# Kernel tuning notes

Measured on AMD Instinct MI355X. Metric: run time of the kernel, lower is better.

Reference implementation:

```python
import jax, jax.numpy as jnp
import numpy as np


def _gru_cell(x, h, Wih, Whh):
    # PyTorch GRU (bias=False): gates ordered [r, z, n] along rows of W.
    gi = x @ Wih.T              # [B, 3H]
    gh = h @ Whh.T              # [B, 3H]
    ir, iz, inn = jnp.split(gi, 3, axis=-1)
    hr, hz, hn = jnp.split(gh, 3, axis=-1)
    r = jax.nn.sigmoid(ir + hr)
    z = jax.nn.sigmoid(iz + hz)
    n = jnp.tanh(inn + r * hn)
    return (1.0 - z) * n + z * h


def setup_inputs() -> dict:
    key = jax.random.key(0)
    ks = jax.random.split(key, 16)
    B, T = 256, 1024
    U, Z, Y, H = 16, 16, 16, 128
    W = 0.1  # weight scale for stable recurrence
    inp = {
        "u": jax.random.normal(ks[0], (B, U, T), jnp.float32),
        "y": jax.random.normal(ks[1], (B, Y, T), jnp.float32),
        "h0": jax.random.uniform(ks[2], (2, B, H), jnp.float32),
        "Wih0": W * jax.random.normal(ks[3], (3 * H, U + Z), jnp.float32),
        "Whh0": W * jax.random.normal(ks[4], (3 * H, H), jnp.float32),
        "Wih1": W * jax.random.normal(ks[5], (3 * H, H), jnp.float32),
        "Whh1": W * jax.random.normal(ks[6], (3 * H, H), jnp.float32),
        "dW1": W * jax.random.normal(ks[7], (H, U + H), jnp.float32),
        "db1": jnp.zeros((H,), jnp.float32),
        "dW2": W * jax.random.normal(ks[8], (Z, H), jnp.float32),
        "db2": jnp.zeros((Z,), jnp.float32),
        "mW1": W * jax.random.normal(ks[9], (H, Z + H), jnp.float32),
        "mb1": jnp.zeros((H,), jnp.float32),
        "mW2": W * jax.random.normal(ks[10], (H, H), jnp.float32),
        "mb2": jnp.zeros((H,), jnp.float32),
        "mW3": W * jax.random.normal(ks[11], (Y, H), jnp.float32),
        "mb3": jnp.zeros((Y,), jnp.float32),
    }
    return inp


def reference(u, y, h0, Wih0, Whh0, Wih1, Whh1,
              dW1, db1, dW2, db2, mW1, mb1, mW2, mb2, mW3, mb3):
    B, Z = u.shape[0], dW2.shape[0]
    u_t = jnp.transpose(u, (2, 0, 1))  # [T, B, U]
    y_t = jnp.transpose(y, (2, 0, 1))  # [T, B, Y]

    def step(carry, xs):
        h, x_prev, loss = carry  # h: [2, B, H]
        ut, yt = xs
        inp = jnp.concatenate([ut, x_prev], axis=1)       # [B, U+Z]
        h0n = _gru_cell(inp, h[0], Wih0, Whh0)
        h1n = _gru_cell(h0n, h[1], Wih1, Whh1)
        h_new = jnp.stack([h0n, h1n], axis=0)
        # dynn: two Linears, no activation; input cat(u_t, h[-1])
        d_in = jnp.concatenate([ut, h1n], axis=1)         # [B, U+H]
        x_t = (d_in @ dW1.T + db1) @ dW2.T + db2          # [B, Z]
        # menn: Linear -> ReLU -> Linear -> Linear; input cat(x_t, h[0])
        m_in = jnp.concatenate([x_t, h0n], axis=1)        # [B, Z+H]
        m = jax.nn.relu(m_in @ mW1.T + mb1)
        m = m @ mW2.T + mb2
        y_hat = m @ mW3.T + mb3                           # [B, Y]
        loss = loss + jnp.sum((y_hat - yt) ** 2)
        return (h_new, x_t, loss), None

    x0 = jnp.zeros((B, Z), jnp.float32)  # x_tm1 at t=0 is zeros
    (_, _, loss), _ = jax.lax.scan(step, (h0, x0, jnp.float32(0.0)), (u_t, y_t))
    return loss
```

## Files before the change

### kernel.cpp

```cpp
#include <hip/hip_runtime.h>

typedef __bf16 bf16x8 __attribute__((ext_vector_type(8)));
typedef float f32x4 __attribute__((ext_vector_type(4)));
typedef unsigned int uint32;
typedef unsigned short u16;

#define T_STEPS 1024
#define CH_STR 784

#define H0_OFF   0
#define H1_OFF   8704
#define M1_OFF   17408
#define UCH_OFF  21760
#define YCH_OFF  46848
#define WL_OFF   71936
#define LDS_BYTES 146688

#define TG0 0
#define TG1 24
#define TG2 120
#define TG3 216
#define TG4 312
#define TG5 317
#define TG6 357
#define NT_TOT 361
#define SC_DC  369664
#define SC_ME  378880
#define SC_DBC 387072
#define SC_MBE 387136

static __device__ __forceinline__ u16 f2bf(float f) {
    uint32 u = __builtin_bit_cast(uint32, f);
    return (u16)((u + 0x7FFFu + ((u >> 16) & 1u)) >> 16);
}
static __device__ __forceinline__ float bf2f(u16 h) {
    uint32 u = ((uint32)h) << 16;
    return __builtin_bit_cast(float, u);
}
static __device__ __forceinline__ uint32 cvtpk(float a, float b) {
    uint32 r;
    asm("v_cvt_pk_bf16_f32 %0, %1, %2" : "=v"(r) : "v"(a), "v"(b));
    return r;
}
static __device__ __forceinline__ float sigm(float x) {
    return __builtin_amdgcn_rcpf(1.f + __builtin_amdgcn_exp2f(x * -1.4426950408889634f));
}
static __device__ __forceinline__ float tanh_fast(float x) {
    float xm = fmaxf(x, -30.f);
    float e = __builtin_amdgcn_exp2f(xm * -2.8853900817779268f);
    return fmaf(2.f, __builtin_amdgcn_rcpf(e + 1.f), -1.f);
}
static __device__ __forceinline__ f32x4 mfma16(bf16x8 a, bf16x8 b, f32x4 c) {
    return __builtin_amdgcn_mfma_f32_16x16x32_bf16(a, b, c, 0, 0, 0);
}
static __device__ __forceinline__ bf16x8 ldsAF(const char* p) {
    return __builtin_bit_cast(bf16x8, *(const uint4*)p);
}

__global__ void prep1(const float* __restrict__ dW1, const float* __restrict__ db1,
                      const float* __restrict__ dW2, const float* __restrict__ db2,
                      const float* __restrict__ mW2, const float* __restrict__ mb2,
                      const float* __restrict__ mW3, const float* __restrict__ mb3,
                      char* __restrict__ ws, float* __restrict__ out) {
    int id = blockIdx.x * 256 + threadIdx.x;
    if (id == 0) *out = 0.f;
    if (id < 2304) {
        int n = id / 144, k = id % 144;
        float s = 0.f;
        for (int h = 0; h < 128; ++h) s += dW2[n * 128 + h] * dW1[h * 144 + k];
        ((float*)(ws + SC_DC))[id] = s;
    } else if (id < 4352) {
        int e = id - 2304, n = e / 128, k = e % 128;
        float s = 0.f;
        for (int h = 0; h < 128; ++h) s += mW3[n * 128 + h] * mW2[h * 128 + k];
        ((float*)(ws + SC_ME))[e] = s;
    } else if (id < 4368) {
        int n = id - 4352;
        float s = db2[n];
        for (int h = 0; h < 128; ++h) s += dW2[n * 128 + h] * db1[h];
        ((float*)(ws + SC_DBC))[n] = s;
    } else if (id < 4384) {
        int n = id - 4368;
        float s = mb3[n];
        for (int h = 0; h < 128; ++h) s += mW3[n * 128 + h] * mb2[h];
        ((float*)(ws + SC_MBE))[n] = s;
    }
}

__global__ void prep2(const float* __restrict__ W0, const float* __restrict__ W1,
                      const float* __restrict__ W2, const float* __restrict__ W3,
                      const float* __restrict__ W5, char* __restrict__ ws) {
    const int tt = blockIdx.x;
    const int lane = threadIdx.x;
    const int cum[8] = {TG0, TG1, TG2, TG3, TG4, TG5, TG6, NT_TOT};
    const int Kreal[7] = {32, 128, 128, 128, 144, 144, 128};
    const int KT[7] = {1, 4, 4, 4, 5, 5, 4};
    const float* Ws[7] = {W0, W1, W2, W3, (const float*)(ws + SC_DC), W5, (const float*)(ws + SC_ME)};
    int g = 0;
    while (tt >= cum[g + 1]) ++g;
    const int tl = tt - cum[g];
    const int kt = tl % KT[g];
    const int n = (tl / KT[g]) * 16 + (lane & 15);
    const float* W = Ws[g];
    u16* o = (u16*)ws + tt * 512 + lane * 8;
#pragma unroll
    for (int j = 0; j < 8; ++j) {
        int k = kt * 32 + (lane >> 4) * 8 + j;
        o[j] = (k < Kreal[g]) ? f2bf(W[n * Kreal[g] + k]) : (u16)0;
    }
}

__global__ __launch_bounds__(512, 2) void rnn_main(
    const float* __restrict__ u, const float* __restrict__ yg, const float* __restrict__ h0g,
    const char* __restrict__ ws, const float* __restrict__ mb1g,
    const float* __restrict__ dbCg, const float* __restrict__ mbEg,
    float* __restrict__ out) {
    __shared__ __align__(16) char smem[LDS_BYTES];
    const int tid = threadIdx.x;
    const int lane = tid & 63;
    const int w = tid >> 6;
    const int lr = lane & 15;
    const int lg = lane >> 4;
    const int r0 = blockIdx.x * 16;
    const uint4* F4 = (const uint4*)ws;
    const f32x4 zero = {0.f, 0.f, 0.f, 0.f};

    for (int i = tid; i < 1024; i += 512) {
        int lay = i >> 9, rem = i & 511, rr = rem >> 5, k4 = rem & 31;
        float4 v = *(const float4*)(h0g + (lay * 256 + r0 + rr) * 128 + k4 * 4);
        uint2 pk;
        pk.x = (uint32)f2bf(v.x) | ((uint32)f2bf(v.y) << 16);
        pk.y = (uint32)f2bf(v.z) | ((uint32)f2bf(v.w) << 16);
        *(uint2*)(smem + H0_OFF + lay * 8704 + rr * 272 + k4 * 8) = pk;
    }
    for (int i = tid; i < 73 * 64; i += 512) {
        int li = i >> 6, ln2 = i & 63;
        int gt2 = (li < 24) ? li : (li < 29) ? TG4 + (li - 24) : (li < 69) ? TG5 + (li - 29) : TG6 + (li - 69);
        *((uint4*)(smem + WL_OFF) + i) = F4[gt2 * 64 + ln2];
    }
    __syncthreads();

    bf16x8 wW[3][3][4];
    for (int p = 0; p < 6; ++p) {
        for (int i = tid; i < 3072; i += 512)
            *((uint4*)(smem + UCH_OFF) + i) = F4[(TG1 + p * 48) * 64 + i];
        __syncthreads();
#pragma unroll
        for (int mat = 0; mat < 3; ++mat)
#pragma unroll
            for (int gg = 0; gg < 3; ++gg) {
                int rel0 = mat * 96 + gg * 32 + w * 4;
                if (rel0 >= p * 48 && rel0 < p * 48 + 48) {
#pragma unroll
                    for (int kt = 0; kt < 4; ++kt)
                        wW[mat][gg][kt] = ldsAF(smem + UCH_OFF + (rel0 - p * 48 + kt) * 1024 + lane * 16);
                }
            }
        __syncthreads();
    }

    const float mb1_c = mb1g[w * 16 + lr];
    const float mbE_l = mbEg[lr];
    float dbc4[4];
#pragma unroll
    for (int i = 0; i < 4; ++i) dbc4[i] = dbCg[lg * 4 + i];
    float hp0[4], hp1[4];
#pragma unroll
    for (int i = 0; i < 4; ++i) {
        hp0[i] = h0g[(r0 + lg * 4 + i) * 128 + w * 16 + lr];
        hp1[i] = h0g[(256 + r0 + lg * 4 + i) * 128 + w * 16 + lr];
    }
    float loss = 0.f;
    const int c2 = (w * 16 + lr) * 2;
    const int bp0 = (lr + (lg & 1) * 32) * 4;

    for (int t = 0; t < T_STEPS; ++t) {
        const char* h0c = smem + H0_OFF + (t & 1) * 4352;
        char* h0n = smem + H0_OFF + ((t & 1) ^ 1) * 4352;
        const char* h1c = smem + H1_OFF + (t & 1) * 4352;
        char* h1n = smem + H1_OFF + ((t & 1) ^ 1) * 4352;
        const int s = t & 31, sp = (t - 1) & 31;
        const char* h1r = h1c + lr * 272;

        bf16x8 ad0 = ldsAF((lg < 2) ? (smem + UCH_OFF + sp * CH_STR + lr * 48 + lg * 16)
                                    : (h1r + (lg - 2) * 16));
        bf16x8 ad1 = ldsAF(h1r + 32 + lg * 16);
        bf16x8 ad2 = ldsAF(h1r + 96 + lg * 16);
        bf16x8 ad3 = ldsAF(h1r + 160 + lg * 16);
        bf16x8 ad4 = ldsAF(h1r + 224 + (lg & 1) * 16);
        f32x4 xa = mfma16(ldsAF(smem + WL_OFF + 24 * 1024 + lane * 16), ad0, zero);
        xa = mfma16(ldsAF(smem + WL_OFF + 25 * 1024 + lane * 16), ad1, xa);
        xa = mfma16(ldsAF(smem + WL_OFF + 26 * 1024 + lane * 16), ad2, xa);
        f32x4 xb = mfma16(ldsAF(smem + WL_OFF + 27 * 1024 + lane * 16), ad3, zero);
        xb = mfma16(ldsAF(smem + WL_OFF + 28 * 1024 + lane * 16), ad4, xb);
        uint32 pk0 = cvtpk(xa[0] + xb[0] + dbc4[0], xa[1] + xb[1] + dbc4[1]);
        uint32 pk1 = cvtpk(xa[2] + xb[2] + dbc4[2], xa[3] + xb[3] + dbc4[3]);
        if (t == 0) { pk0 = 0u; pk1 = 0u; }
        uint32 d0 = (uint32)__builtin_amdgcn_ds_bpermute(bp0, (int)pk0);
        uint32 d1 = (uint32)__builtin_amdgcn_ds_bpermute(bp0, (int)pk1);
        uint32 d2 = (uint32)__builtin_amdgcn_ds_bpermute(bp0 + 64, (int)pk0);
        uint32 d3 = (uint32)__builtin_amdgcn_ds_bpermute(bp0 + 64, (int)pk1);
        bf16x8 xfrag = __builtin_bit_cast(bf16x8, (uint4){d0, d1, d2, d3});

        if ((t & 31) == 0) {
            __syncthreads();
#pragma unroll
            for (int it = 0; it < 8; ++it) {
                int g = it * 16 + (tid >> 5);
                int rr2 = g >> 3, chp = g & 7, ss = lane & 31;
                const float* up = u + (r0 + rr2) * 16384 + (2 * chp) * 1024 + t + ss;
                *(uint32*)(smem + UCH_OFF + ss * CH_STR + rr2 * 48 + chp * 4) =
                    cvtpk(up[0], up[1024]);
                int gt = t - 1 + ss;
                const float* yp = yg + (r0 + rr2) * 16384 + (2 * chp) * 1024 + gt;
                uint32 py = (gt >= 0) ? cvtpk(yp[0], yp[1024]) : 0u;
                *(uint32*)(smem + YCH_OFF + ss * CH_STR + rr2 * 48 + chp * 4) = py;
            }
            __syncthreads();
        }

        bf16x8 ufrag = ldsAF(smem + UCH_OFF + s * CH_STR + lr * 48 + (lg & 1) * 16);
        bf16x8 a_inp = (lg < 2) ? ufrag : xfrag;
        const char* h0r = h0c + lr * 272;
        bf16x8 ah0 = ldsAF(h0r + lg * 16);
        bf16x8 ah1 = ldsAF(h0r + 64 + lg * 16);
        bf16x8 ah2 = ldsAF(h0r + 128 + lg * 16);
        bf16x8 ah3 = ldsAF(h0r + 192 + lg * 16);
        bf16x8 b0r = ldsAF(smem + WL_OFF + (0 * 8 + w) * 1024 + lane * 16);
        bf16x8 b0z = ldsAF(smem + WL_OFF + (1 * 8 + w) * 1024 + lane * 16);
        bf16x8 b0n = ldsAF(smem + WL_OFF + (2 * 8 + w) * 1024 + lane * 16);
        f32x4 rA = mfma16(ah0, wW[0][0][0], zero);
        rA = mfma16(ah1, wW[0][0][1], rA);
        rA = mfma16(a_inp, b0r, rA);
        f32x4 rB = mfma16(ah2, wW[0][0][2], zero);
        rB = mfma16(ah3, wW[0][0][3], rB);
        f32x4 zA = mfma16(ah0, wW[0][1][0], zero);
        zA = mfma16(ah1, wW[0][1][1], zA);
        zA = mfma16(a_inp, b0z, zA);
        f32x4 zB = mfma16(ah2, wW[0][1][2], zero);
        zB = mfma16(ah3, wW[0][1][3], zB);
        f32x4 nI = mfma16(a_inp, b0n, zero);
        f32x4 nA = mfma16(ah0, wW[0][2][0], zero);
        nA = mfma16(ah1, wW[0][2][1], nA);
        f32x4 nB = mfma16(ah2, wW[0][2][2], zero);
        nB = mfma16(ah3, wW[0][2][3], nB);
        bf16x8 am0 = (lg < 2) ? xfrag : ldsAF(h0r + (lg - 2) * 16);
        bf16x8 am1 = ldsAF(h0r + 32 + lg * 16);
        bf16x8 am2 = ldsAF(h0r + 96 + lg * 16);
        bf16x8 am3 = ldsAF(h0r + 160 + lg * 16);
        bf16x8 am4 = ldsAF(h0r + 224 + (lg & 1) * 16);
        const int mb = 29 + w * 5;
        f32x4 mA = mfma16(am1, ldsAF(smem + WL_OFF + (mb + 1) * 1024 + lane * 16), zero);
        mA = mfma16(am2, ldsAF(smem + WL_OFF + (mb + 2) * 1024 + lane * 16), mA);
        mA = mfma16(am0, ldsAF(smem + WL_OFF + (mb + 0) * 1024 + lane * 16), mA);
        f32x4 mB = mfma16(am3, ldsAF(smem + WL_OFF + (mb + 3) * 1024 + lane * 16), zero);
        mB = mfma16(am4, ldsAF(smem + WL_OFF + (mb + 4) * 1024 + lane * 16), mB);
#pragma unroll
        for (int i = 0; i < 4; ++i) {
            float rr = sigm(rA[i] + rB[i]);
            float zz = sigm(zA[i] + zB[i]);
            float nn = tanh_fast(fmaf(rr, nA[i] + nB[i], nI[i]));
            float hnew = fmaf(zz, hp0[i] - nn, nn);
            hp0[i] = hnew;
            *(u16*)(h0n + (lg * 4 + i) * 272 + c2) = (u16)cvtpk(hnew, hnew);
            float mv = fmaxf(mA[i] + mB[i] + mb1_c, 0.f);
            *(u16*)(smem + M1_OFF + (lg * 4 + i) * 272 + c2) = (u16)cvtpk(mv, mv);
        }
        __syncthreads();

        const char* h0nr = h0n + lr * 272;
        bf16x8 ag0 = ldsAF(h0nr + lg * 16);
        bf16x8 ag1 = ldsAF(h0nr + 64 + lg * 16);
        bf16x8 ag2 = ldsAF(h0nr + 128 + lg * 16);
        bf16x8 ag3 = ldsAF(h0nr + 192 + lg * 16);
        bf16x8 av0 = ldsAF(h1r + lg * 16);
        bf16x8 av1 = ldsAF(h1r + 64 + lg * 16);
        bf16x8 av2 = ldsAF(h1r + 128 + lg * 16);
        bf16x8 av3 = ldsAF(h1r + 192 + lg * 16);
        bf16x8 q0, q1, q2, q3, we0, we1, we2, we3;
        if (w == 7) {
            const char* m1r = smem + M1_OFF + lr * 272;
            q0 = ldsAF(m1r + lg * 16);
            q1 = ldsAF(m1r + 64 + lg * 16);
            q2 = ldsAF(m1r + 128 + lg * 16);
            q3 = ldsAF(m1r + 192 + lg * 16);
            we0 = ldsAF(smem + WL_OFF + 69 * 1024 + lane * 16);
            we1 = ldsAF(smem + WL_OFF + 70 * 1024 + lane * 16);
            we2 = ldsAF(smem + WL_OFF + 71 * 1024 + lane * 16);
            we3 = ldsAF(smem + WL_OFF + 72 * 1024 + lane * 16);
        }
        f32x4 bRi = mfma16(ag0, wW[1][0][0], zero);
        bRi = mfma16(ag1, wW[1][0][1], bRi);
        bRi = mfma16(ag2, wW[1][0][2], bRi);
        bRi = mfma16(ag3, wW[1][0][3], bRi);
        f32x4 bRh = mfma16(av0, wW[2][0][0], zero);
        bRh = mfma16(av1, wW[2][0][1], bRh);
        bRh = mfma16(av2, wW[2][0][2], bRh);
        bRh = mfma16(av3, wW[2][0][3], bRh);
        f32x4 bZi = mfma16(ag0, wW[1][1][0], zero);
        bZi = mfma16(ag1, wW[1][1][1], bZi);
        bZi = mfma16(ag2, wW[1][1][2], bZi);
        bZi = mfma16(ag3, wW[1][1][3], bZi);
        f32x4 bZh = mfma16(av0, wW[2][1][0], zero);
        bZh = mfma16(av1, wW[2][1][1], bZh);
        bZh = mfma16(av2, wW[2][1][2], bZh);
        bZh = mfma16(av3, wW[2][1][3], bZh);
        f32x4 bNi = mfma16(ag0, wW[1][2][0], zero);
        bNi = mfma16(ag1, wW[1][2][1], bNi);
        bNi = mfma16(ag2, wW[1][2][2], bNi);
        bNi = mfma16(ag3, wW[1][2][3], bNi);
        f32x4 bNh = mfma16(av0, wW[2][2][0], zero);
        bNh = mfma16(av1, wW[2][2][1], bNh);
        bNh = mfma16(av2, wW[2][2][2], bNh);
        bNh = mfma16(av3, wW[2][2][3], bNh);
        if (w == 7) {
            f32x4 lA = mfma16(q0, we0, zero);
            lA = mfma16(q1, we1, lA);
            f32x4 lB = mfma16(q2, we2, zero);
            lB = mfma16(q3, we3, lB);
            const float gd = (t > 0) ? 1.f : 0.f;
#pragma unroll
            for (int i = 0; i < 4; ++i) {
                float yh = lA[i] + lB[i] + mbE_l;
                float yv = bf2f(*(const u16*)(smem + YCH_OFF + s * CH_STR + (lg * 4 + i) * 48 + lr * 2));
                float d = yh - yv;
                loss = fmaf(gd * d, d, loss);
            }
        }
#pragma unroll
        for (int i = 0; i < 4; ++i) {
            float rr = sigm(bRi[i] + bRh[i]);
            float zz = sigm(bZi[i] + bZh[i]);
            float nn = tanh_fast(fmaf(rr, bNh[i], bNi[i]));
            float hnew = fmaf(zz, hp1[i] - nn, nn);
            hp1[i] = hnew;
            *(u16*)(h1n + (lg * 4 + i) * 272 + c2) = (u16)cvtpk(hnew, hnew);
        }
        __syncthreads();
    }

    {
        const char* h0c = smem + H0_OFF;
        const char* h1c = smem + H1_OFF;
        const char* h1r = h1c + lr * 272;
        const char* h0r = h0c + lr * 272;
        bf16x8 ad0 = ldsAF((lg < 2) ? (smem + UCH_OFF + 31 * CH_STR + lr * 48 + lg * 16)
                                    : (h1r + (lg - 2) * 16));
        bf16x8 ad1 = ldsAF(h1r + 32 + lg * 16);
        bf16x8 ad2 = ldsAF(h1r + 96 + lg * 16);
        bf16x8 ad3 = ldsAF(h1r + 160 + lg * 16);
        bf16x8 ad4 = ldsAF(h1r + 224 + (lg & 1) * 16);
        f32x4 xa = mfma16(ldsAF(smem + WL_OFF + 24 * 1024 + lane * 16), ad0, zero);
        xa = mfma16(ldsAF(smem + WL_OFF + 25 * 1024 + lane * 16), ad1, xa);
        xa = mfma16(ldsAF(smem + WL_OFF + 26 * 1024 + lane * 16), ad2, xa);
        f32x4 xb = mfma16(ldsAF(smem + WL_OFF + 27 * 1024 + lane * 16), ad3, zero);
        xb = mfma16(ldsAF(smem + WL_OFF + 28 * 1024 + lane * 16), ad4, xb);
        uint32 pk0 = cvtpk(xa[0] + xb[0] + dbc4[0], xa[1] + xb[1] + dbc4[1]);
        uint32 pk1 = cvtpk(xa[2] + xb[2] + dbc4[2], xa[3] + xb[3] + dbc4[3]);
        uint32 d0 = (uint32)__builtin_amdgcn_ds_bpermute(bp0, (int)pk0);
        uint32 d1 = (uint32)__builtin_amdgcn_ds_bpermute(bp0, (int)pk1);
        uint32 d2 = (uint32)__builtin_amdgcn_ds_bpermute(bp0 + 64, (int)pk0);
        uint32 d3 = (uint32)__builtin_amdgcn_ds_bpermute(bp0 + 64, (int)pk1);
        bf16x8 xfrag = __builtin_bit_cast(bf16x8, (uint4){d0, d1, d2, d3});
        bf16x8 am0 = (lg < 2) ? xfrag : ldsAF(h0r + (lg - 2) * 16);
        bf16x8 am1 = ldsAF(h0r + 32 + lg * 16);
        bf16x8 am2 = ldsAF(h0r + 96 + lg * 16);
        bf16x8 am3 = ldsAF(h0r + 160 + lg * 16);
        bf16x8 am4 = ldsAF(h0r + 224 + (lg & 1) * 16);
        const int mb = 29 + w * 5;
        f32x4 m = mfma16(am0, ldsAF(smem + WL_OFF + (mb + 0) * 1024 + lane * 16), zero);
        m = mfma16(am1, ldsAF(smem + WL_OFF + (mb + 1) * 1024 + lane * 16), m);
        m = mfma16(am2, ldsAF(smem + WL_OFF + (mb + 2) * 1024 + lane * 16), m);
        m = mfma16(am3, ldsAF(smem + WL_OFF + (mb + 3) * 1024 + lane * 16), m);
        m = mfma16(am4, ldsAF(smem + WL_OFF + (mb + 4) * 1024 + lane * 16), m);
#pragma unroll
        for (int i = 0; i < 4; ++i) {
            float mv = fmaxf(m[i] + mb1_c, 0.f);
            *(u16*)(smem + M1_OFF + (lg * 4 + i) * 272 + c2) = (u16)cvtpk(mv, mv);
        }
        __syncthreads();
        if (w == 7) {
            const char* m1r = smem + M1_OFF + lr * 272;
            bf16x8 q0 = ldsAF(m1r + lg * 16);
            bf16x8 q1 = ldsAF(m1r + 64 + lg * 16);
            bf16x8 q2 = ldsAF(m1r + 128 + lg * 16);
            bf16x8 q3 = ldsAF(m1r + 192 + lg * 16);
            f32x4 lA = mfma16(q0, ldsAF(smem + WL_OFF + 69 * 1024 + lane * 16), zero);
            lA = mfma16(q1, ldsAF(smem + WL_OFF + 70 * 1024 + lane * 16), lA);
            f32x4 lB = mfma16(q2, ldsAF(smem + WL_OFF + 71 * 1024 + lane * 16), zero);
            lB = mfma16(q3, ldsAF(smem + WL_OFF + 72 * 1024 + lane * 16), lB);
#pragma unroll
            for (int i = 0; i < 4; ++i) {
                float yh = lA[i] + lB[i] + mbE_l;
                float yv = yg[(r0 + lg * 4 + i) * 16384 + lr * 1024 + 1023];
                float d = yh - yv;
                loss = fmaf(d, d, loss);
            }
        }
    }

    if (w == 7) {
#pragma unroll
        for (int off = 32; off > 0; off >>= 1) loss += __shfl_down(loss, off, 64);
        if (lane == 0) atomicAdd(out, loss);
    }
}

extern "C" void kernel_launch(void* const* d_in, const int* in_sizes, int n_in,
                              void* d_out, int out_size, void* d_ws, size_t ws_size,
                              hipStream_t stream) {
    const float* u    = (const float*)d_in[0];
    const float* y    = (const float*)d_in[1];
    const float* h0   = (const float*)d_in[2];
    const float* Wih0 = (const float*)d_in[3];
    const float* Whh0 = (const float*)d_in[4];
    const float* Wih1 = (const float*)d_in[5];
    const float* Whh1 = (const float*)d_in[6];
    const float* dW1  = (const float*)d_in[7];
    const float* db1  = (const float*)d_in[8];
    const float* dW2  = (const float*)d_in[9];
    const float* db2  = (const float*)d_in[10];
    const float* mW1  = (const float*)d_in[11];
    const float* mb1  = (const float*)d_in[12];
    const float* mW2  = (const float*)d_in[13];
    const float* mb2  = (const float*)d_in[14];
    const float* mW3  = (const float*)d_in[15];
    const float* mb3  = (const float*)d_in[16];
    float* out = (float*)d_out;
    char* ws = (char*)d_ws;

    prep1<<<dim3(18), dim3(256), 0, stream>>>(dW1, db1, dW2, db2, mW2, mb2, mW3, mb3, ws, out);
    prep2<<<dim3(NT_TOT), dim3(64), 0, stream>>>(Wih0, Whh0, Wih1, Whh1, mW1, ws);
    rnn_main<<<dim3(16), dim3(512), 0, stream>>>(u, y, h0, ws, mb1,
                                                 (const float*)(ws + SC_DBC),
                                                 (const float*)(ws + SC_MBE), out);
}
```

Baseline: 3.053 ms.

## Swap MFMA operand order to produce transposed outputs and vectorize LDS stores

Swaps the A/B operands of every MFMA so each lane's four accumulator values fall along the hidden dimension for one batch row instead of along the batch dimension. This lets the new h0, h1 and menn hidden values be packed into a single 8-byte LDS store per lane rather than four scalar 2-byte stores. Biases and the initial hidden state are loaded as float4 to match the new mapping, and the y chunk loss read becomes one vector load. The u/y chunk staging loop is rewritten to store one bf16 per element with a tighter stride of 768, which adds more global loads and narrower stores in the refill every 32 steps.

Result: slower. 4.439 ms (+45.4%).

```diff
diff --git a/kernel.cpp b/kernel.cpp
--- a/kernel.cpp
+++ b/kernel.cpp
@@ -6,15 +6,15 @@
 typedef unsigned short u16;
 
 #define T_STEPS 1024
-#define CH_STR 784
+#define CH_STR 768
 
 #define H0_OFF   0
 #define H1_OFF   8704
 #define M1_OFF   17408
 #define UCH_OFF  21760
-#define YCH_OFF  46848
-#define WL_OFF   71936
-#define LDS_BYTES 146688
+#define YCH_OFF  46336
+#define WL_OFF   70912
+#define LDS_BYTES 145664
 
 #define TG0 0
 #define TG1 24
@@ -159,20 +159,31 @@
         __syncthreads();
     }
 
-    const float mb1_c = mb1g[w * 16 + lr];
-    const float mbE_l = mbEg[lr];
-    float dbc4[4];
-#pragma unroll
-    for (int i = 0; i < 4; ++i) dbc4[i] = dbCg[lg * 4 + i];
+    float mb1_4[4], dbc4[4], mbe4[4];
+    {
+        float4 t1 = *(const float4*)(mb1g + w * 16 + lg * 4);
+        float4 t2 = *(const float4*)(dbCg + lg * 4);
+        float4 t3 = *(const float4*)(mbEg + lg * 4);
+#pragma unroll
+        for (int i = 0; i < 4; ++i) {
+            mb1_4[i] = ((const float*)&t1)[i];
+            dbc4[i] = ((const float*)&t2)[i];
+            mbe4[i] = ((const float*)&t3)[i];
+        }
+    }
     float hp0[4], hp1[4];
-#pragma unroll
-    for (int i = 0; i < 4; ++i) {
-        hp0[i] = h0g[(r0 + lg * 4 + i) * 128 + w * 16 + lr];
-        hp1[i] = h0g[(256 + r0 + lg * 4 + i) * 128 + w * 16 + lr];
+    {
+        float4 t1 = *(const float4*)(h0g + (r0 + lr) * 128 + w * 16 + lg * 4);
+        float4 t2 = *(const float4*)(h0g + (256 + r0 + lr) * 128 + w * 16 + lg * 4);
+#pragma unroll
+        for (int i = 0; i < 4; ++i) {
+            hp0[i] = ((const float*)&t1)[i];
+            hp1[i] = ((const float*)&t2)[i];
+        }
     }
     float loss = 0.f;
-    const int c2 = (w * 16 + lr) * 2;
-    const int bp0 = (lr + (lg & 1) * 32) * 4;
+    const int cb = w * 32 + lg * 8;
+    const int bp0 = ((lg & 1) * 32 + lr) * 4;
 
     for (int t = 0; t < T_STEPS; ++t) {
         const char* h0c = smem + H0_OFF + (t & 1) * 4352;
@@ -204,17 +215,16 @@
 
         if ((t & 31) == 0) {
             __syncthreads();
-#pragma unroll
-            for (int it = 0; it < 8; ++it) {
-                int g = it * 16 + (tid >> 5);
-                int rr2 = g >> 3, chp = g & 7, ss = lane & 31;
-                const float* up = u + (r0 + rr2) * 16384 + (2 * chp) * 1024 + t + ss;
-                *(uint32*)(smem + UCH_OFF + ss * CH_STR + rr2 * 48 + chp * 4) =
-                    cvtpk(up[0], up[1024]);
+            for (int q = 0; q < 16; ++q) {
+                int pair = w * 32 + q * 2 + (lane >> 5);
+                int rr2 = pair >> 4, ch = pair & 15, ss = lane & 31;
+                float v = u[(r0 + rr2) * 16384 + ch * 1024 + t + ss];
+                *(u16*)(smem + UCH_OFF + ss * CH_STR + rr2 * 48 + ch * 2) = f2bf(v);
                 int gt = t - 1 + ss;
-                const float* yp = yg + (r0 + rr2) * 16384 + (2 * chp) * 1024 + gt;
-                uint32 py = (gt >= 0) ? cvtpk(yp[0], yp[1024]) : 0u;
-                *(uint32*)(smem + YCH_OFF + ss * CH_STR + rr2 * 48 + chp * 4) = py;
+                if (gt >= 0) {
+                    float vy = yg[(r0 + rr2) * 16384 + ch * 1024 + gt];
+                    *(u16*)(smem + YCH_OFF + ss * CH_STR + rr2 * 48 + ch * 2) = f2bf(vy);
+                }
             }
             __syncthreads();
         }
@@ -229,42 +239,50 @@
         bf16x8 b0r = ldsAF(smem + WL_OFF + (0 * 8 + w) * 1024 + lane * 16);
         bf16x8 b0z = ldsAF(smem + WL_OFF + (1 * 8 + w) * 1024 + lane * 16);
         bf16x8 b0n = ldsAF(smem + WL_OFF + (2 * 8 + w) * 1024 + lane * 16);
-        f32x4 rA = mfma16(ah0, wW[0][0][0], zero);
-        rA = mfma16(ah1, wW[0][0][1], rA);
-        rA = mfma16(a_inp, b0r, rA);
-        f32x4 rB = mfma16(ah2, wW[0][0][2], zero);
-        rB = mfma16(ah3, wW[0][0][3], rB);
-        f32x4 zA = mfma16(ah0, wW[0][1][0], zero);
-        zA = mfma16(ah1, wW[0][1][1], zA);
-        zA = mfma16(a_inp, b0z, zA);
-        f32x4 zB = mfma16(ah2, wW[0][1][2], zero);
-        zB = mfma16(ah3, wW[0][1][3], zB);
-        f32x4 nI = mfma16(a_inp, b0n, zero);
-        f32x4 nA = mfma16(ah0, wW[0][2][0], zero);
-        nA = mfma16(ah1, wW[0][2][1], nA);
-        f32x4 nB = mfma16(ah2, wW[0][2][2], zero);
-        nB = mfma16(ah3, wW[0][2][3], nB);
+        f32x4 rA = mfma16(wW[0][0][0], ah0, zero);
+        rA = mfma16(wW[0][0][1], ah1, rA);
+        rA = mfma16(b0r, a_inp, rA);
+        f32x4 rB = mfma16(wW[0][0][2], ah2, zero);
+        rB = mfma16(wW[0][0][3], ah3, rB);
+        f32x4 zA = mfma16(wW[0][1][0], ah0, zero);
+        zA = mfma16(wW[0][1][1], ah1, zA);
+        zA = mfma16(b0z, a_inp, zA);
+        f32x4 zB = mfma16(wW[0][1][2], ah2, zero);
+        zB = mfma16(wW[0][1][3], ah3, zB);
+        f32x4 nI = mfma16(b0n, a_inp, zero);
+        f32x4 nA = mfma16(wW[0][2][0], ah0, zero);
+        nA = mfma16(wW[0][2][1], ah1, nA);
+        f32x4 nB = mfma16(wW[0][2][2], ah2, zero);
+        nB = mfma16(wW[0][2][3], ah3, nB);
         bf16x8 am0 = (lg < 2) ? xfrag : ldsAF(h0r + (lg - 2) * 16);
         bf16x8 am1 = ldsAF(h0r + 32 + lg * 16);
         bf16x8 am2 = ldsAF(h0r + 96 + lg * 16);
         bf16x8 am3 = ldsAF(h0r + 160 + lg * 16);
         bf16x8 am4 = ldsAF(h0r + 224 + (lg & 1) * 16);
         const int mb = 29 + w * 5;
-        f32x4 mA = mfma16(am1, ldsAF(smem + WL_OFF + (mb + 1) * 1024 + lane * 16), zero);
-        mA = mfma16(am2, ldsAF(smem + WL_OFF + (mb + 2) * 1024 + lane * 16), mA);
-        mA = mfma16(am0, ldsAF(smem + WL_OFF + (mb + 0) * 1024 + lane * 16), mA);
-        f32x4 mB = mfma16(am3, ldsAF(smem + WL_OFF + (mb + 3) * 1024 + lane * 16), zero);
-        mB = mfma16(am4, ldsAF(smem + WL_OFF + (mb + 4) * 1024 + lane * 16), mB);
+        f32x4 mA = mfma16(ldsAF(smem + WL_OFF + (mb + 1) * 1024 + lane * 16), am1, zero);
+        mA = mfma16(ldsAF(smem + WL_OFF + (mb + 2) * 1024 + lane * 16), am2, mA);
+        mA = mfma16(ldsAF(smem + WL_OFF + (mb + 0) * 1024 + lane * 16), am0, mA);
+        f32x4 mB = mfma16(ldsAF(smem + WL_OFF + (mb + 3) * 1024 + lane * 16), am3, zero);
+        mB = mfma16(ldsAF(smem + WL_OFF + (mb + 4) * 1024 + lane * 16), am4, mB);
+        float hn0[4];
 #pragma unroll
         for (int i = 0; i < 4; ++i) {
             float rr = sigm(rA[i] + rB[i]);
             float zz = sigm(zA[i] + zB[i]);
             float nn = tanh_fast(fmaf(rr, nA[i] + nB[i], nI[i]));
-            float hnew = fmaf(zz, hp0[i] - nn, nn);
-            hp0[i] = hnew;
-            *(u16*)(h0n + (lg * 4 + i) * 272 + c2) = (u16)cvtpk(hnew, hnew);
-            float mv = fmaxf(mA[i] + mB[i] + mb1_c, 0.f);
-            *(u16*)(smem + M1_OFF + (lg * 4 + i) * 272 + c2) = (u16)cvtpk(mv, mv);
+            hn0[i] = fmaf(zz, hp0[i] - nn, nn);
+            hp0[i] = hn0[i];
+        }
+        {
+            uint2 hv = {cvtpk(hn0[0], hn0[1]), cvtpk(hn0[2], hn0[3])};
+            *(uint2*)(h0n + lr * 272 + cb) = hv;
+            float m0 = fmaxf(mA[0] + mB[0] + mb1_4[0], 0.f);
+            float m1v = fmaxf(mA[1] + mB[1] + mb1_4[1], 0.f);
+            float m2v = fmaxf(mA[2] + mB[2] + mb1_4[2], 0.f);
+            float m3v = fmaxf(mA[3] + mB[3] + mb1_4[3], 0.f);
+            uint2 mv = {cvtpk(m0, m1v), cvtpk(m2v, m3v)};
+            *(uint2*)(smem + M1_OFF + lr * 272 + cb) = mv;
         }
         __syncthreads();
 
@@ -289,52 +307,57 @@
             we2 = ldsAF(smem + WL_OFF + 71 * 1024 + lane * 16);
             we3 = ldsAF(smem + WL_OFF + 72 * 1024 + lane * 16);
         }
-        f32x4 bRi = mfma16(ag0, wW[1][0][0], zero);
-        bRi = mfma16(ag1, wW[1][0][1], bRi);
-        bRi = mfma16(ag2, wW[1][0][2], bRi);
-        bRi = mfma16(ag3, wW[1][0][3], bRi);
-        f32x4 bRh = mfma16(av0, wW[2][0][0], zero);
-        bRh = mfma16(av1, wW[2][0][1], bRh);
-        bRh = mfma16(av2, wW[2][0][2], bRh);
-        bRh = mfma16(av3, wW[2][0][3], bRh);
-        f32x4 bZi = mfma16(ag0, wW[1][1][0], zero);
-        bZi = mfma16(ag1, wW[1][1][1], bZi);
-        bZi = mfma16(ag2, wW[1][1][2], bZi);
-        bZi = mfma16(ag3, wW[1][1][3], bZi);
-        f32x4 bZh = mfma16(av0, wW[2][1][0], zero);
-        bZh = mfma16(av1, wW[2][1][1], bZh);
-        bZh = mfma16(av2, wW[2][1][2], bZh);
-        bZh = mfma16(av3, wW[2][1][3], bZh);
-        f32x4 bNi = mfma16(ag0, wW[1][2][0], zero);
-        bNi = mfma16(ag1, wW[1][2][1], bNi);
-        bNi = mfma16(ag2, wW[1][2][2], bNi);
-        bNi = mfma16(ag3, wW[1][2][3], bNi);
-        f32x4 bNh = mfma16(av0, wW[2][2][0], zero);
-        bNh = mfma16(av1, wW[2][2][1], bNh);
-        bNh = mfma16(av2, wW[2][2][2], bNh);
-        bNh = mfma16(av3, wW[2][2][3], bNh);
+        f32x4 bRi = mfma16(wW[1][0][0], ag0, zero);
+        bRi = mfma16(wW[1][0][1], ag1, bRi);
+        bRi = mfma16(wW[1][0][2], ag2, bRi);
+        bRi = mfma16(wW[1][0][3], ag3, bRi);
+        f32x4 bRh = mfma16(wW[2][0][0], av0, zero);
+        bRh = mfma16(wW[2][0][1], av1, bRh);
+        bRh = mfma16(wW[2][0][2], av2, bRh);
+        bRh = mfma16(wW[2][0][3], av3, bRh);
+        f32x4 bZi = mfma16(wW[1][1][0], ag0, zero);
+        bZi = mfma16(wW[1][1][1], ag1, bZi);
+        bZi = mfma16(wW[1][1][2], ag2, bZi);
+        bZi = mfma16(wW[1][1][3], ag3, bZi);
+        f32x4 bZh = mfma16(wW[2][1][0], av0, zero);
+        bZh = mfma16(wW[2][1][1], av1, bZh);
+        bZh = mfma16(wW[2][1][2], av2, bZh);
+        bZh = mfma16(wW[2][1][3], av3, bZh);
+        f32x4 bNi = mfma16(wW[1][2][0], ag0, zero);
+        bNi = mfma16(wW[1][2][1], ag1, bNi);
+        bNi = mfma16(wW[1][2][2], ag2, bNi);
+        bNi = mfma16(wW[1][2][3], ag3, bNi);
+        f32x4 bNh = mfma16(wW[2][2][0], av0, zero);
+        bNh = mfma16(wW[2][2][1], av1, bNh);
+        bNh = mfma16(wW[2][2][2], av2, bNh);
+        bNh = mfma16(wW[2][2][3], av3, bNh);
         if (w == 7) {
-            f32x4 lA = mfma16(q0, we0, zero);
-            lA = mfma16(q1, we1, lA);
-            f32x4 lB = mfma16(q2, we2, zero);
-            lB = mfma16(q3, we3, lB);
+            f32x4 lA = mfma16(we0, q0, zero);
+            lA = mfma16(we1, q1, lA);
+            f32x4 lB = mfma16(we2, q2, zero);
+            lB = mfma16(we3, q3, lB);
             const float gd = (t > 0) ? 1.f : 0.f;
+            uint2 yv2 = *(const uint2*)(smem + YCH_OFF + s * CH_STR + lr * 48 + lg * 8);
 #pragma unroll
             for (int i = 0; i < 4; ++i) {
-                float yh = lA[i] + lB[i] + mbE_l;
-                float yv = bf2f(*(const u16*)(smem + YCH_OFF + s * CH_STR + (lg * 4 + i) * 48 + lr * 2));
-                float d = yh - yv;
+                float yh = lA[i] + lB[i] + mbe4[i];
+                u16 yb = (u16)(((const u16*)&yv2)[i]);
+                float d = yh - bf2f(yb);
                 loss = fmaf(gd * d, d, loss);
             }
         }
+        float hn1[4];
 #pragma unroll
         for (int i = 0; i < 4; ++i) {
             float rr = sigm(bRi[i] + bRh[i]);
             float zz = sigm(bZi[i] + bZh[i]);
             float nn = tanh_fast(fmaf(rr, bNh[i], bNi[i]));
-            float hnew = fmaf(zz, hp1[i] - nn, nn);
-            hp1[i] = hnew;
-            *(u16*)(h1n + (lg * 4 + i) * 272 + c2) = (u16)cvtpk(hnew, hnew);
+            hn1[i] = fmaf(zz, hp1[i] - nn, nn);
+            hp1[i] = hn1[i];
+        }
+        {
+            uint2 hv = {cvtpk(hn1[0], hn1[1]), cvtpk(hn1[2], hn1[3])};
+            *(uint2*)(h1n + lr * 272 + cb) = hv;
         }
         __syncthreads();
     }
@@ -368,15 +391,18 @@
         bf16x8 am3 = ldsAF(h0r + 160 + lg * 16);
         bf16x8 am4 = ldsAF(h0r + 224 + (lg & 1) * 16);
         const int mb = 29 + w * 5;
-        f32x4 m = mfma16(am0, ldsAF(smem + WL_OFF + (mb + 0) * 1024 + lane * 16), zero);
-        m = mfma16(am1, ldsAF(smem + WL_OFF + (mb + 1) * 1024 + lane * 16), m);
-        m = mfma16(am2, ldsAF(smem + WL_OFF + (mb + 2) * 1024 + lane * 16), m);
-        m = mfma16(am3, ldsAF(smem + WL_OFF + (mb + 3) * 1024 + lane * 16), m);
-        m = mfma16(am4, ldsAF(smem + WL_OFF + (mb + 4) * 1024 + lane * 16), m);
-#pragma unroll
-        for (int i = 0; i < 4; ++i) {
-            float mv = fmaxf(m[i] + mb1_c, 0.f);
-            *(u16*)(smem + M1_OFF + (lg * 4 + i) * 272 + c2) = (u16)cvtpk(mv, mv);
+        f32x4 m = mfma16(ldsAF(smem + WL_OFF + (mb + 0) * 1024 + lane * 16), am0, zero);
+        m = mfma16(ldsAF(smem + WL_OFF + (mb + 1) * 1024 + lane * 16), am1, m);
+        m = mfma16(ldsAF(smem + WL_OFF + (mb + 2) * 1024 + lane * 16), am2, m);
+        m = mfma16(ldsAF(smem + WL_OFF + (mb + 3) * 1024 + lane * 16), am3, m);
+        m = mfma16(ldsAF(smem + WL_OFF + (mb + 4) * 1024 + lane * 16), am4, m);
+        {
+            float m0 = fmaxf(m[0] + mb1_4[0], 0.f);
+            float m1v = fmaxf(m[1] + mb1_4[1], 0.f);
+            float m2v = fmaxf(m[2] + mb1_4[2], 0.f);
+            float m3v = fmaxf(m[3] + mb1_4[3], 0.f);
+            uint2 mv = {cvtpk(m0, m1v), cvtpk(m2v, m3v)};
+            *(uint2*)(smem + M1_OFF + lr * 272 + cb) = mv;
         }
         __syncthreads();
         if (w == 7) {
@@ -385,14 +411,14 @@
             bf16x8 q1 = ldsAF(m1r + 64 + lg * 16);
             bf16x8 q2 = ldsAF(m1r + 128 + lg * 16);
             bf16x8 q3 = ldsAF(m1r + 192 + lg * 16);
-            f32x4 lA = mfma16(q0, ldsAF(smem + WL_OFF + 69 * 1024 + lane * 16), zero);
-            lA = mfma16(q1, ldsAF(smem + WL_OFF + 70 * 1024 + lane * 16), lA);
-            f32x4 lB = mfma16(q2, ldsAF(smem + WL_OFF + 71 * 1024 + lane * 16), zero);
-            lB = mfma16(q3, ldsAF(smem + WL_OFF + 72 * 1024 + lane * 16), lB);
+            f32x4 lA = mfma16(ldsAF(smem + WL_OFF + 69 * 1024 + lane * 16), q0, zero);
+            lA = mfma16(ldsAF(smem + WL_OFF + 70 * 1024 + lane * 16), q1, lA);
+            f32x4 lB = mfma16(ldsAF(smem + WL_OFF + 71 * 1024 + lane * 16), q2, zero);
+            lB = mfma16(ldsAF(smem + WL_OFF + 72 * 1024 + lane * 16), q3, lB);
 #pragma unroll
             for (int i = 0; i < 4; ++i) {
-                float yh = lA[i] + lB[i] + mbE_l;
-                float yv = yg[(r0 + lg * 4 + i) * 16384 + lr * 1024 + 1023];
+                float yh = lA[i] + lB[i] + mbe4[i];
+                float yv = yg[(r0 + lr) * 16384 + (lg * 4 + i) * 1024 + 1023];
                 float d = yh - yv;
                 loss = fmaf(d, d, loss);
             }
```
